# Kernel optimization log

Measured on AMD Instinct MI355X. Metric: run time of the kernel, lower is better.

The kernel has to match this reference:

```python
import jax, jax.numpy as jnp
import numpy as np

EPS = 1e-5

def setup_inputs() -> dict:
    key = jax.random.key(0)
    k1, k2, k3 = jax.random.split(key, 3)
    x = jax.random.normal(k1, (16, 256, 32, 32), dtype=jnp.float32)
    embed = jax.random.normal(k2, (8192, 256), dtype=jnp.float32)
    cluster_size = jax.random.uniform(k3, (8192,), dtype=jnp.float32)
    return {"x": x, "embed": embed, "cluster_size": cluster_size}

def reference(x, embed, cluster_size):
    # x: (b, c, h, w) -> (b, h*w, c); project_in is Identity (codebook_dim == dim, heads=1)
    b, c, h, w = x.shape
    xt = jnp.transpose(x, (0, 2, 3, 1)).reshape(b, h * w, c)   # (b, n, d)
    flat = xt.reshape(-1, c)                                    # (N, d)
    d2 = (jnp.sum(flat * flat, axis=1, keepdims=True)
          - 2.0 * flat @ embed.T
          + jnp.sum(embed * embed, axis=1))                     # (N, K)
    embed_ind_flat = jnp.argmin(d2, axis=-1)                    # (N,) temperature==0 -> argmax of -d2
    quantize = embed[embed_ind_flat].reshape(b, h * w, c)       # gather codebook rows
    embed_ind = embed_ind_flat.reshape(b, h * w)
    # perplexity over (unnormalized) EMA cluster sizes, as in the torch code
    probs = cluster_size
    perplexity = jnp.exp(-jnp.sum(probs * jnp.log(probs + EPS)))
    # eval-mode commitment loss (weight_loss=True, commitment_weight=1.0)
    commit_loss = jnp.mean((quantize - xt) ** 2)
    return quantize, embed_ind, perplexity, commit_loss
```

## Files before the change

kernel.cpp:

```cpp
#include <hip/hip_runtime.h>
#include <hip/hip_bf16.h>
#include <math.h>

typedef _Float16 f16x8 __attribute__((ext_vector_type(8)));
typedef float f32x4 __attribute__((ext_vector_type(4)));

#define N_TOK 16384
#define D 256
#define K 8192

#define Q_OFF 0
#define IND_OFF 4194304
#define PERP_OFF 4210688
#define COMMIT_OFF 4210689

#define WS_CAND   0u
#define WS_E2     1048576u
#define WS_DSUM   1081344u
#define WS_EH     1114112u
#define WS_XH     5308416u
#define WS_XT     13697024u
#define WS_NEED   30474240u

__device__ __forceinline__ unsigned int ford(float f) {
    unsigned int u = __float_as_uint(f);
    return (u & 0x80000000u) ? ~u : (u | 0x80000000u);
}
__device__ __forceinline__ unsigned short f2h(float f) {
    _Float16 h = (_Float16)f;
    return *(unsigned short*)&h;
}


__global__ void vq_convert_x(const float* __restrict__ x, float* __restrict__ xt,
                             unsigned short* __restrict__ xh) {
    __shared__ float t[64][65];
    const int tid = threadIdx.x;
    const int p0 = blockIdx.x * 64, c0 = blockIdx.y * 64, b = blockIdx.z;
    const int q = tid & 15, h = tid >> 4;
    #pragma unroll
    for (int r = 0; r < 4; ++r) {
        const int cl = r * 16 + h;
        const float4 v = *(const float4*)(x + (((size_t)(b * 256 + c0 + cl)) << 10) + p0 + q * 4);
        t[cl][q * 4 + 0] = v.x; t[cl][q * 4 + 1] = v.y;
        t[cl][q * 4 + 2] = v.z; t[cl][q * 4 + 3] = v.w;
    }
    __syncthreads();
    #pragma unroll
    for (int r = 0; r < 4; ++r) {
        const int nl = r * 16 + h;
        const int n = (b << 10) + p0 + nl;
        const int c = c0 + q * 4;
        float4 vf; ushort4 vh;
        vf.x = t[q * 4 + 0][nl]; vf.y = t[q * 4 + 1][nl];
        vf.z = t[q * 4 + 2][nl]; vf.w = t[q * 4 + 3][nl];
        vh.x = f2h(vf.x); vh.y = f2h(vf.y); vh.z = f2h(vf.z); vh.w = f2h(vf.w);
        *(float4*)(xt + ((size_t)n << 8) + c) = vf;
        *(ushort4*)(xh + ((size_t)n << 8) + c) = vh;
    }
}

__global__ void vq_prep_e(const float* __restrict__ e, unsigned short* __restrict__ ehT,
                          float* __restrict__ e2, double* __restrict__ dsum) {
    if (blockIdx.x == 0 && threadIdx.x == 0) *dsum = 0.0;
    const int wave = threadIdx.x >> 6, lane = threadIdx.x & 63;
    const int c = blockIdx.x * 4 + wave;
    const float4 v = *(const float4*)(e + (size_t)c * D + lane * 4);
    ushort4 vh;
    vh.x = f2h(v.x); vh.y = f2h(v.y); vh.z = f2h(v.z); vh.w = f2h(v.w);
    unsigned short* dst = ehT + (((size_t)(c >> 4)) << 12) + ((lane >> 1) << 7) +
                          ((c & 15) << 3) + ((lane & 1) << 2);
    *(ushort4*)dst = vh;
    float s = v.x * v.x + v.y * v.y + v.z * v.z + v.w * v.w;
    #pragma unroll
    for (int off = 32; off > 0; off >>= 1) s += __shfl_down(s, off, 64);
    if (lane == 0) e2[c] = s;
}

__global__ __launch_bounds__(256)
void vq_mfma_kernel(
    const unsigned short* __restrict__ xh, const unsigned short* __restrict__ ehT,
    const float* __restrict__ e2, unsigned int* __restrict__ cand) {
    __shared__ float e2s[1024];

    const int tid = threadIdx.x;
    const int lane = tid & 63, wid = tid >> 6;
    const int l15 = lane & 15, lg = lane >> 4;
    const int split = blockIdx.y;
    const int m0 = blockIdx.x * 256;
    const int c0s = split * 1024;
    const int rw = m0 + wid * 64;

    *(float4*)&e2s[tid * 4] = *(const float4*)(e2 + c0s + tid * 4);

    f16x8 a[4][8];
    #pragma unroll
    for (int mf = 0; mf < 4; ++mf) {
        const unsigned short* ap = xh + (((size_t)(rw + mf * 16 + l15)) << 8) + lg * 8;
        #pragma unroll
        for (int t = 0; t < 8; ++t)
            a[mf][t] = *(const f16x8*)(ap + t * 32);
    }
    __syncthreads();

    const char* bb = (const char*)ehT + (((size_t)c0s) << 9) + lane * 16;

    float d1[16], d2[16];
    unsigned int ipk[16];
    #pragma unroll
    for (int r = 0; r < 16; ++r) { d1[r] = INFINITY; d2[r] = INFINITY; ipk[r] = 0; }

    #pragma unroll 1
    for (int tile = 0; tile < 64; ++tile) {
        const char* tb = bb + tile * 8192;
        f16x8 b[8];
        #pragma unroll
        for (int j = 0; j < 8; ++j) b[j] = *(const f16x8*)(tb + j * 1024);
        const float e2v = e2s[tile * 16 + l15];
        f32x4 acc[4];
        #pragma unroll
        for (int mf = 0; mf < 4; ++mf) {
            f32x4 z = {0.f, 0.f, 0.f, 0.f};
            acc[mf] = z;
        }
        #pragma unroll
        for (int j = 0; j < 8; ++j)
            #pragma unroll
            for (int mf = 0; mf < 4; ++mf)
                acc[mf] = __builtin_amdgcn_mfma_f32_16x16x32_f16(
                    a[mf][j], b[j], acc[mf], 0, 0, 0);
        const unsigned int cl = (unsigned int)(tile * 16 + l15);
        #pragma unroll
        for (int mf = 0; mf < 4; ++mf)
            #pragma unroll
            for (int reg = 0; reg < 4; ++reg) {
                const int rr = mf * 4 + reg;
                const float s = fmaf(-2.0f, acc[mf][reg], e2v);
                if (s < d2[rr]) {
                    const bool lt1 = s < d1[rr];
                    const unsigned int ii = ipk[rr];
                    d2[rr] = lt1 ? d1[rr] : s;
                    ipk[rr] = lt1 ? ((ii << 16) | cl) : ((ii & 0xFFFFu) | (cl << 16));
                    d1[rr] = lt1 ? s : d1[rr];
                }
            }
    }

    unsigned long long p1[16], p2[16];
    #pragma unroll
    for (int r = 0; r < 16; ++r) {
        p1[r] = (((unsigned long long)ford(d1[r])) << 32) |
                (unsigned int)(c0s + (ipk[r] & 0xFFFFu));
        p2[r] = (((unsigned long long)ford(d2[r])) << 32) |
                (unsigned int)(c0s + (ipk[r] >> 16));
    }
    #pragma unroll
    for (int st = 1; st < 16; st <<= 1) {
        #pragma unroll
        for (int r = 0; r < 16; ++r) {
            const unsigned long long q1 = __shfl_xor(p1[r], st, 64);
            const unsigned long long q2 = __shfl_xor(p2[r], st, 64);
            const unsigned long long n1 = p1[r] < q1 ? p1[r] : q1;
            const unsigned long long hi = p1[r] < q1 ? q1 : p1[r];
            const unsigned long long l2 = p2[r] < q2 ? p2[r] : q2;
            p1[r] = n1;
            p2[r] = hi < l2 ? hi : l2;
        }
    }
    if (l15 == 0) {
        #pragma unroll
        for (int mf = 0; mf < 4; ++mf)
            #pragma unroll
            for (int reg = 0; reg < 4; ++reg) {
                const int n = rw + mf * 16 + lg * 4 + reg;
                unsigned int* cp = cand + (((size_t)n) << 4) + split * 2;
                cp[0] = (unsigned int)p1[mf * 4 + reg];
                cp[1] = (unsigned int)p2[mf * 4 + reg];
            }
    }
}

__global__ void vq_rescore_finalize(const float* __restrict__ xt, const float* __restrict__ embed,
                                    const float* __restrict__ e2,
                                    const unsigned int* __restrict__ cand,
                                    float* __restrict__ out, double* __restrict__ dsum) {
    __shared__ double red[4];
    const int tid = threadIdx.x, wid = tid >> 6, lane = tid & 63;
    double wsum = 0.0;
    #pragma unroll 1
    for (int it = 0; it < 8; ++it) {
        const int n = blockIdx.x * 32 + it * 4 + wid;
        const float4 xv = *(const float4*)(xt + (((size_t)n) << 8) + lane * 4);
        unsigned long long best = 0xFFFFFFFFFFFFFFFFull;
        #pragma unroll 2
        for (int j = 0; j < 16; ++j) {
            const unsigned int c = cand[(((size_t)n) << 4) + j];
            const float4 ev = *(const float4*)(embed + (((size_t)c) << 8) + lane * 4);
            float dt = xv.x * ev.x + xv.y * ev.y + xv.z * ev.z + xv.w * ev.w;
            #pragma unroll
            for (int off = 32; off > 0; off >>= 1) dt += __shfl_xor(dt, off, 64);
            const float s = fmaf(-2.0f, dt, e2[c]);
            const unsigned long long p = (((unsigned long long)ford(s)) << 32) | c;
            best = p < best ? p : best;
        }
        const unsigned int bi = (unsigned int)(best & 0xFFFFFFFFull);
        if (lane == 0) out[IND_OFF + n] = (float)bi;
        const float4 ev = *(const float4*)(embed + (((size_t)bi) << 8) + lane * 4);
        *(float4*)(out + Q_OFF + (((size_t)n) << 8) + lane * 4) = ev;
        const float q0 = ev.x - xv.x, q1 = ev.y - xv.y, q2 = ev.z - xv.z, q3 = ev.w - xv.w;
        float a4 = q0 * q0 + q1 * q1 + q2 * q2 + q3 * q3;
        #pragma unroll
        for (int off = 32; off > 0; off >>= 1) a4 += __shfl_xor(a4, off, 64);
        if (lane == 0) wsum += (double)a4;
    }
    if (lane == 0) red[wid] = wsum;
    __syncthreads();
    if (tid == 0) atomicAdd(dsum, red[0] + red[1] + red[2] + red[3]);
}

__global__ void vq_tail_kernel(const float* __restrict__ cs,
                               const double* __restrict__ dsum,
                               float* __restrict__ out) {
    __shared__ double red[4];
    const int tid = threadIdx.x;
    double s = 0.0;
    for (int i = tid; i < K; i += 256) {
        const float p = cs[i];
        s += (double)(p * logf(p + 1e-5f));
    }
    #pragma unroll
    for (int off = 32; off > 0; off >>= 1) s += __shfl_down(s, off, 64);
    if ((tid & 63) == 0) red[tid >> 6] = s;
    __syncthreads();
    if (tid == 0) {
        const double tot = red[0] + red[1] + red[2] + red[3];
        const double pv = exp(-tot);
        out[PERP_OFF] = (pv > 3.3e38) ? 3.3e38f : (float)pv;
        out[COMMIT_OFF] = (float)(*dsum * (1.0 / 4194304.0));
    }
}

#define TM 64
#define TN 64
#define BKF 32
#define NSPLITF 2
#define CODES_PER_SPLIT (K / NSPLITF)
#define TILES_PER_SPLIT (CODES_PER_SPLIT / TN)

__global__ void vq_init_kernel(unsigned long long* __restrict__ keys, double* __restrict__ dsum) {
    int i = blockIdx.x * blockDim.x + threadIdx.x;
    if (i < N_TOK) keys[i] = 0xFFFFFFFFFFFFFFFFull;
    if (i == 0) *dsum = 0.0;
}
__global__ void vq_e2_kernel(const float* __restrict__ embed, float* __restrict__ e2) {
    int wave = threadIdx.x >> 6, lane = threadIdx.x & 63;
    int c = blockIdx.x * 4 + wave;
    const float4 v = *(const float4*)(embed + (size_t)c * D + lane * 4);
    float s = v.x * v.x + v.y * v.y + v.z * v.z + v.w * v.w;
    #pragma unroll
    for (int off = 32; off > 0; off >>= 1) s += __shfl_down(s, off, 64);
    if (lane == 0) e2[c] = s;
}
__global__ __launch_bounds__(256, 2) void vq_argmin_kernel(
    const float* __restrict__ x, const float* __restrict__ embed,
    const float* __restrict__ e2, unsigned long long* __restrict__ keys) {
    __shared__ float xT[D][TM];
    __shared__ float eT[BKF][TN + 4];
    const int tid = threadIdx.x;
    const int n0 = blockIdx.x * TM;
    const int b = n0 >> 10, p0 = n0 & 1023;
    const float* xb = x + (size_t)b * D * 1024 + p0;
    {
        const int t4 = (tid & 15) * 4, chb = tid >> 4;
        #pragma unroll
        for (int pass = 0; pass < 16; ++pass) {
            const int ch = pass * 16 + chb;
            *(float4*)&xT[ch][t4] = *(const float4*)(xb + (size_t)ch * 1024 + t4);
        }
    }
    __syncthreads();
    const int tm4 = (tid & 15) * 4, tn = tid >> 4, tn4 = tn * 4;
    float bestd[4]; int besti[4];
    #pragma unroll
    for (int i = 0; i < 4; ++i) { bestd[i] = INFINITY; besti[i] = 0x7fffffff; }
    for (int ct = 0; ct < TILES_PER_SPLIT; ++ct) {
        const int c0 = blockIdx.y * CODES_PER_SPLIT + ct * TN;
        float acc[4][4] = {};
        for (int kk = 0; kk < D; kk += BKF) {
            {
                const int j = tid >> 2, ch4 = (tid & 3) * 4;
                #pragma unroll
                for (int p = 0; p < 2; ++p) {
                    const int chl = p * 16 + ch4;
                    const float4 ev = *(const float4*)(embed + (size_t)(c0 + j) * D + kk + chl);
                    eT[chl + 0][j] = ev.x; eT[chl + 1][j] = ev.y;
                    eT[chl + 2][j] = ev.z; eT[chl + 3][j] = ev.w;
                }
            }
            __syncthreads();
            #pragma unroll
            for (int k2 = 0; k2 < BKF; ++k2) {
                const float4 a = *(const float4*)&xT[kk + k2][tm4];
                const float4 bv = *(const float4*)&eT[k2][tn4];
                acc[0][0] += a.x * bv.x; acc[0][1] += a.x * bv.y; acc[0][2] += a.x * bv.z; acc[0][3] += a.x * bv.w;
                acc[1][0] += a.y * bv.x; acc[1][1] += a.y * bv.y; acc[1][2] += a.y * bv.z; acc[1][3] += a.y * bv.w;
                acc[2][0] += a.z * bv.x; acc[2][1] += a.z * bv.y; acc[2][2] += a.z * bv.z; acc[2][3] += a.z * bv.w;
                acc[3][0] += a.w * bv.x; acc[3][1] += a.w * bv.y; acc[3][2] += a.w * bv.z; acc[3][3] += a.w * bv.w;
            }
            __syncthreads();
        }
        #pragma unroll
        for (int j = 0; j < 4; ++j) {
            const int c = c0 + tn4 + j;
            const float ec = e2[c];
            #pragma unroll
            for (int i = 0; i < 4; ++i) {
                const float s = ec - 2.0f * acc[i][j];
                if (s < bestd[i]) { bestd[i] = s; besti[i] = c; }
            }
        }
    }
    __syncthreads();
    float* cd = &eT[0][0];
    int* ci = (int*)&eT[16][0];
    #pragma unroll
    for (int i = 0; i < 4; ++i) { cd[tn * 64 + tm4 + i] = bestd[i]; ci[tn * 64 + tm4 + i] = besti[i]; }
    __syncthreads();
    if (tid < TM) {
        float bd = INFINITY; int bi = 0x7fffffff;
        for (int j = 0; j < 16; ++j) {
            const float d = cd[j * 64 + tid]; const int idx = ci[j * 64 + tid];
            if (d < bd || (d == bd && idx < bi)) { bd = d; bi = idx; }
        }
        atomicMin(&keys[n0 + tid], (((unsigned long long)ford(bd)) << 32) | (unsigned int)bi);
    }
}
__global__ void vq_finalize_kernel(const float* __restrict__ x, const float* __restrict__ embed,
                                   const unsigned long long* __restrict__ keys,
                                   float* __restrict__ out, double* __restrict__ dsum) {
    const int tid = threadIdx.x;
    const int n0 = blockIdx.x * 64;
    const int t = tid >> 2, q = tid & 3;
    const int n = n0 + t;
    const int b = n >> 10, p = n & 1023;
    if (tid < 64) {
        const int nn = n0 + tid;
        out[IND_OFF + nn] = (float)(int)(unsigned int)(keys[nn] & 0xFFFFFFFFull);
    }
    const int idx = (int)(unsigned int)(keys[n] & 0xFFFFFFFFull);
    const float* erow = embed + (size_t)idx * D;
    const float* xrow = x + (size_t)b * D * 1024 + p;
    float* qrow = out + Q_OFF + (size_t)n * D;
    float acc = 0.0f;
    #pragma unroll
    for (int i = 0; i < 16; ++i) {
        const int ch = i * 16 + q * 4;
        const float4 ev = *(const float4*)(erow + ch);
        *(float4*)(qrow + ch) = ev;
        const float x0 = xrow[(size_t)(ch + 0) * 1024];
        const float x1 = xrow[(size_t)(ch + 1) * 1024];
        const float x2 = xrow[(size_t)(ch + 2) * 1024];
        const float x3 = xrow[(size_t)(ch + 3) * 1024];
        const float d0 = ev.x - x0, d1 = ev.y - x1, d2 = ev.z - x2, d3 = ev.w - x3;
        acc += d0 * d0 + d1 * d1 + d2 * d2 + d3 * d3;
    }
    #pragma unroll
    for (int off = 32; off > 0; off >>= 1) acc += __shfl_down(acc, off, 64);
    if ((tid & 63) == 0) atomicAdd(dsum, (double)acc);
}

extern "C" void kernel_launch(void* const* d_in, const int* in_sizes, int n_in,
                              void* d_out, int out_size, void* d_ws, size_t ws_size,
                              hipStream_t stream) {
    const float* x = (const float*)d_in[0];
    const float* embed = (const float*)d_in[1];
    const float* cs = (const float*)d_in[2];
    float* out = (float*)d_out;
    char* ws = (char*)d_ws;

    if (ws_size >= (size_t)WS_NEED) {
        unsigned int* cand = (unsigned int*)(ws + WS_CAND);
        float* e2 = (float*)(ws + WS_E2);
        double* dsum = (double*)(ws + WS_DSUM);
        unsigned short* ehT = (unsigned short*)(ws + WS_EH);
        unsigned short* xh = (unsigned short*)(ws + WS_XH);
        float* xt = (float*)(ws + WS_XT);

        vq_prep_e<<<dim3(K / 4), dim3(256), 0, stream>>>(embed, ehT, e2, dsum);
        vq_convert_x<<<dim3(16, 4, 16), dim3(256), 0, stream>>>(x, xt, xh);
        vq_mfma_kernel<<<dim3(64, 8), dim3(256), 0, stream>>>(xh, ehT, e2, cand);
        vq_rescore_finalize<<<dim3(512), dim3(256), 0, stream>>>(xt, embed, e2, cand, out, dsum);
        vq_tail_kernel<<<dim3(1), dim3(256), 0, stream>>>(cs, dsum, out);
    } else {
        unsigned long long* keys = (unsigned long long*)ws;
        float* e2 = (float*)(ws + 131072);
        double* dsum = (double*)(ws + 163840);
        vq_init_kernel<<<dim3(64), dim3(256), 0, stream>>>(keys, dsum);
        vq_e2_kernel<<<dim3(K / 4), dim3(256), 0, stream>>>(embed, e2);
        vq_argmin_kernel<<<dim3(N_TOK / TM, NSPLITF), dim3(256), 0, stream>>>(x, embed, e2, keys);
        vq_finalize_kernel<<<dim3(256), dim3(256), 0, stream>>>(x, embed, keys, out, dsum);
        vq_tail_kernel<<<dim3(1), dim3(256), 0, stream>>>(cs, dsum, out);
    }
}
```

Before: 196.4 us.

## Double-buffer codebook tiles and pack top-2 distance+index into 32-bit keys

The candidate-search loop now processes two tiles per iteration with two B-register buffers and two accumulator sets. The next tile's loads and the previous tile's top-2 epilogue can then overlap the MFMA work of the current tile. The branchy top-2 update with separate float and index arrays is replaced by branchless min/max on 32-bit keys: the order-preserving float bits with the low 10 bits overwritten by the local column index. Reductions also drop from 64-bit to 32-bit shuffles. This costs more registers, which may lower occupancy. Truncating the distance mantissa can pick wrong near-tie candidates, which the exact rescoring pass is expected to correct.

Result: faster. 171.8 us (-12.5%).

```diff
diff --git a/kernel.cpp b/kernel.cpp
--- a/kernel.cpp
+++ b/kernel.cpp
@@ -105,79 +105,95 @@
 
     const char* bb = (const char*)ehT + (((size_t)c0s) << 9) + lane * 16;
 
-    float d1[16], d2[16];
-    unsigned int ipk[16];
-    #pragma unroll
-    for (int r = 0; r < 16; ++r) { d1[r] = INFINITY; d2[r] = INFINITY; ipk[r] = 0; }
-
+    unsigned int p1[16], p2[16];
+    #pragma unroll
+    for (int r = 0; r < 16; ++r) { p1[r] = 0xFFFFFFFFu; p2[r] = 0xFFFFFFFFu; }
+
+    f16x8 bA[8], bB[8];
+    f32x4 accA[4], accB[4];
+
+#define LOADT(breg, t)                                            \
+    {                                                             \
+        const char* tb_ = bb + (t) * 8192;                        \
+        _Pragma("unroll")                                         \
+        for (int j_ = 0; j_ < 8; ++j_)                            \
+            breg[j_] = *(const f16x8*)(tb_ + j_ * 1024);          \
+    }
+
+#define MFMAT(acc, breg)                                          \
+    {                                                             \
+        _Pragma("unroll")                                         \
+        for (int mf_ = 0; mf_ < 4; ++mf_) {                       \
+            f32x4 z_ = {0.f, 0.f, 0.f, 0.f};                      \
+            acc[mf_] = z_;                                        \
+        }                                                         \
+        _Pragma("unroll")                                         \
+        for (int j_ = 0; j_ < 8; ++j_)                            \
+            _Pragma("unroll")                                     \
+            for (int mf_ = 0; mf_ < 4; ++mf_)                     \
+                acc[mf_] = __builtin_amdgcn_mfma_f32_16x16x32_f16(\
+                    a[mf_][j_], breg[j_], acc[mf_], 0, 0, 0);     \
+    }
+
+#define EPI(acc, tile)                                                        \
+    {                                                                         \
+        const float e2v_ = e2s[(tile) * 16 + l15];                            \
+        const unsigned int cl_ = (unsigned int)((tile) * 16 + l15);           \
+        _Pragma("unroll")                                                     \
+        for (int mf_ = 0; mf_ < 4; ++mf_)                                     \
+            _Pragma("unroll")                                                 \
+            for (int rg_ = 0; rg_ < 4; ++rg_) {                               \
+                const int rr_ = mf_ * 4 + rg_;                                \
+                const float s_ = fmaf(-2.0f, acc[mf_][rg_], e2v_);            \
+                unsigned int u_ = __float_as_uint(s_);                        \
+                u_ ^= ((unsigned int)((int)u_ >> 31)) | 0x80000000u;          \
+                const unsigned int sp_ = (u_ & 0xFFFFFC00u) | cl_;            \
+                const unsigned int hi_ = p1[rr_] > sp_ ? p1[rr_] : sp_;       \
+                p1[rr_] = p1[rr_] < sp_ ? p1[rr_] : sp_;                      \
+                p2[rr_] = p2[rr_] < hi_ ? p2[rr_] : hi_;                      \
+            }                                                                 \
+    }
+
+    LOADT(bA, 0);
     #pragma unroll 1
-    for (int tile = 0; tile < 64; ++tile) {
-        const char* tb = bb + tile * 8192;
-        f16x8 b[8];
-        #pragma unroll
-        for (int j = 0; j < 8; ++j) b[j] = *(const f16x8*)(tb + j * 1024);
-        const float e2v = e2s[tile * 16 + l15];
-        f32x4 acc[4];
-        #pragma unroll
-        for (int mf = 0; mf < 4; ++mf) {
-            f32x4 z = {0.f, 0.f, 0.f, 0.f};
-            acc[mf] = z;
-        }
-        #pragma unroll
-        for (int j = 0; j < 8; ++j)
-            #pragma unroll
-            for (int mf = 0; mf < 4; ++mf)
-                acc[mf] = __builtin_amdgcn_mfma_f32_16x16x32_f16(
-                    a[mf][j], b[j], acc[mf], 0, 0, 0);
-        const unsigned int cl = (unsigned int)(tile * 16 + l15);
+    for (int t = 0; t < 64; t += 2) {
+        LOADT(bB, t + 1);
+        MFMAT(accA, bA);
+        if (t > 0) EPI(accB, t - 1);
+        if (t + 2 < 64) LOADT(bA, t + 2);
+        MFMAT(accB, bB);
+        EPI(accA, t);
+    }
+    EPI(accB, 63);
+
+    #pragma unroll
+    for (int st = 1; st < 16; st <<= 1) {
+        #pragma unroll
+        for (int r = 0; r < 16; ++r) {
+            const unsigned int q1 = (unsigned int)__shfl_xor((int)p1[r], st, 64);
+            const unsigned int q2 = (unsigned int)__shfl_xor((int)p2[r], st, 64);
+            const unsigned int n1 = p1[r] < q1 ? p1[r] : q1;
+            const unsigned int hi = p1[r] < q1 ? q1 : p1[r];
+            const unsigned int m2 = p2[r] < q2 ? p2[r] : q2;
+            p1[r] = n1;
+            p2[r] = m2 < hi ? m2 : hi;
+        }
+    }
+    if (l15 == 0) {
         #pragma unroll
         for (int mf = 0; mf < 4; ++mf)
             #pragma unroll
             for (int reg = 0; reg < 4; ++reg) {
                 const int rr = mf * 4 + reg;
-                const float s = fmaf(-2.0f, acc[mf][reg], e2v);
-                if (s < d2[rr]) {
-                    const bool lt1 = s < d1[rr];
-                    const unsigned int ii = ipk[rr];
-                    d2[rr] = lt1 ? d1[rr] : s;
-                    ipk[rr] = lt1 ? ((ii << 16) | cl) : ((ii & 0xFFFFu) | (cl << 16));
-                    d1[rr] = lt1 ? s : d1[rr];
-                }
-            }
-    }
-
-    unsigned long long p1[16], p2[16];
-    #pragma unroll
-    for (int r = 0; r < 16; ++r) {
-        p1[r] = (((unsigned long long)ford(d1[r])) << 32) |
-                (unsigned int)(c0s + (ipk[r] & 0xFFFFu));
-        p2[r] = (((unsigned long long)ford(d2[r])) << 32) |
-                (unsigned int)(c0s + (ipk[r] >> 16));
-    }
-    #pragma unroll
-    for (int st = 1; st < 16; st <<= 1) {
-        #pragma unroll
-        for (int r = 0; r < 16; ++r) {
-            const unsigned long long q1 = __shfl_xor(p1[r], st, 64);
-            const unsigned long long q2 = __shfl_xor(p2[r], st, 64);
-            const unsigned long long n1 = p1[r] < q1 ? p1[r] : q1;
-            const unsigned long long hi = p1[r] < q1 ? q1 : p1[r];
-            const unsigned long long l2 = p2[r] < q2 ? p2[r] : q2;
-            p1[r] = n1;
-            p2[r] = hi < l2 ? hi : l2;
-        }
-    }
-    if (l15 == 0) {
-        #pragma unroll
-        for (int mf = 0; mf < 4; ++mf)
-            #pragma unroll
-            for (int reg = 0; reg < 4; ++reg) {
                 const int n = rw + mf * 16 + lg * 4 + reg;
                 unsigned int* cp = cand + (((size_t)n) << 4) + split * 2;
-                cp[0] = (unsigned int)p1[mf * 4 + reg];
-                cp[1] = (unsigned int)p2[mf * 4 + reg];
+                cp[0] = (unsigned int)(c0s + (p1[rr] & 0x3FFu));
+                cp[1] = (unsigned int)(c0s + (p2[rr] & 0x3FFu));
             }
     }
+#undef LOADT
+#undef MFMAT
+#undef EPI
 }
 
 __global__ void vq_rescore_finalize(const float* __restrict__ xt, const float* __restrict__ embed,
```
